# Kernel tuning notes

Measured on AMD Instinct MI355X. Metric: run time of the kernel, lower is better.

The kernel has to match this reference:

```python
import jax, jax.numpy as jnp
import numpy as np

LEAKY_SLOPE = 0.2  # alpha in the torch module
EPS = 1e-10

N_NODES = 100000
N_EDGES = 1600000
IN_F = 128
OUT_F = 64


def setup_inputs() -> dict:
    key = jax.random.key(0)
    k1, k2, k3, k4, k5 = jax.random.split(key, 5)
    h = jax.random.normal(k1, (N_NODES, IN_F), dtype=jnp.float32)
    W = jax.random.normal(k2, (IN_F, OUT_F), dtype=jnp.float32) * (1.0 / np.sqrt(IN_F))
    a1 = jax.random.normal(k3, (OUT_F,), dtype=jnp.float32) * 0.1
    a2 = jax.random.normal(k4, (OUT_F,), dtype=jnp.float32) * 0.1
    edge_index = jax.random.randint(k5, (2, N_EDGES), 0, N_NODES, dtype=jnp.int32)
    return {"h": h, "W": W, "a1": a1, "a2": a2, "edge_index": edge_index}


def reference(h, W, a1, a2, edge_index):
    # h: [N, in_f], W: [in_f, out_f], a1/a2: [out_f], edge_index: [2, E]
    N = h.shape[0]
    Wh = h @ W                                   # [N, out_f]
    row, col = edge_index[0], edge_index[1]      # [E]
    f1 = Wh @ a1                                 # [N]
    f2 = Wh @ a2                                 # [N]
    e = jax.nn.leaky_relu(f1[row] + f2[col], negative_slope=LEAKY_SLOPE)  # [E]
    e_exp = jnp.exp(e - jnp.max(e))              # global-max shift, as in torch code
    exp_sum = jax.ops.segment_sum(e_exp, row, num_segments=N)            # [N]
    alpha = e_exp / (exp_sum[row] + EPS)         # [E]  (dropout is identity in eval)
    weighted_Wh = Wh[col] * alpha[:, None]       # [E, out_f]
    h_prime = jax.ops.segment_sum(weighted_Wh, row, num_segments=N)      # [N, out_f]
    return jax.nn.elu(h_prime)                   # concat=True path
```

## Files before the change

kernel.cpp:

```cpp
#include <hip/hip_runtime.h>
#include <hip/hip_bf16.h>

#define N_NODES 100000
#define N_EDGES 1600000
#define IN_F 128
#define OUT_F 64

#define RPB 64
#define NB  1563
#define C_CHUNKS 250
#define CHUNK 6400
#define M_CNT (NB * C_CHUNKS)
#define SCANA_BLOCKS ((M_CNT + 1023) / 1024)

typedef __attribute__((ext_vector_type(8))) short short8;
typedef __attribute__((ext_vector_type(4))) float f32x4;

#define LDS_PITCH 136

__device__ __forceinline__ unsigned short f2bf(float x) {
    unsigned u = __float_as_uint(x);
    return (unsigned short)((u + 0x7FFFu + ((u >> 16) & 1u)) >> 16);
}
__device__ __forceinline__ float bf2f_u(unsigned short b) {
    return __uint_as_float((unsigned)b << 16);
}

__global__ __launch_bounds__(1024) void k_hist(
    const int* __restrict__ ei, int* __restrict__ cnt,
    const float* __restrict__ W, const float* __restrict__ a1,
    const float* __restrict__ a2, float* __restrict__ wa1, float* __restrict__ wa2)
{
    __shared__ int hl[NB];
    const int c = blockIdx.x;
    if (c == C_CHUNKS) {
        const int k = threadIdx.x;
        if (k < IN_F) {
            float s1 = 0.f, s2 = 0.f;
            #pragma unroll 8
            for (int f = 0; f < OUT_F; f++) {
                const float w = W[k * OUT_F + f];
                s1 += w * a1[f];
                s2 += w * a2[f];
            }
            wa1[k] = s1;
            wa2[k] = s2;
        }
        return;
    }
    for (int i = threadIdx.x; i < NB; i += 1024) hl[i] = 0;
    __syncthreads();
    const int e0 = c * CHUNK;
    for (int i = threadIdx.x; i < CHUNK; i += 1024)
        atomicAdd(&hl[ei[e0 + i] >> 6], 1);
    __syncthreads();
    for (int b = threadIdx.x; b < NB; b += 1024)
        cnt[b * C_CHUNKS + c] = hl[b];
}

__global__ __launch_bounds__(256) void k_gemm(
    const float* __restrict__ h, const float* __restrict__ W,
    const float* __restrict__ wa1, const float* __restrict__ wa2,
    unsigned short* __restrict__ Whb, float* __restrict__ f1, float* __restrict__ f2)
{
    __shared__ unsigned short Wt[OUT_F * LDS_PITCH];
    __shared__ unsigned short Al[16 * LDS_PITCH];

    const int tid  = threadIdx.x;
    const int lane = tid & 63;
    const int wav  = tid >> 6;
    const int quad = lane >> 4;
    const int nl   = lane & 15;

    for (int i = tid; i < IN_F * OUT_F; i += 256) {
        const int k = i >> 6, f = i & 63;
        Wt[f * LDS_PITCH + k] = f2bf(W[i]);
    }
    __syncthreads();

    short8 bfrag[4];
    #pragma unroll
    for (int ch = 0; ch < 4; ch++)
        bfrag[ch] = *(const short8*)&Wt[(wav * 16 + nl) * LDS_PITCH + ch * 32 + quad * 8];

    const int srow = tid >> 4;
    const int sc   = tid & 15;
    float w1r[8], w2r[8];
    #pragma unroll
    for (int j = 0; j < 8; j++) { w1r[j] = wa1[sc * 8 + j]; w2r[j] = wa2[sc * 8 + j]; }

    const int ntiles = N_NODES / 16;
    for (int tile = blockIdx.x; tile < ntiles; tile += gridDim.x) {
        const int base = tile * 16;
        __syncthreads();

        const float4 v0 = *(const float4*)&h[(base + srow) * IN_F + sc * 8];
        const float4 v1 = *(const float4*)&h[(base + srow) * IN_F + sc * 8 + 4];
        float p1 = v0.x * w1r[0] + v0.y * w1r[1] + v0.z * w1r[2] + v0.w * w1r[3]
                 + v1.x * w1r[4] + v1.y * w1r[5] + v1.z * w1r[6] + v1.w * w1r[7];
        float p2 = v0.x * w2r[0] + v0.y * w2r[1] + v0.z * w2r[2] + v0.w * w2r[3]
                 + v1.x * w2r[4] + v1.y * w2r[5] + v1.z * w2r[6] + v1.w * w2r[7];
        #pragma unroll
        for (int m = 8; m >= 1; m >>= 1) {
            p1 += __shfl_xor(p1, m, 64);
            p2 += __shfl_xor(p2, m, 64);
        }
        if (sc == 0) { f1[base + srow] = p1; f2[base + srow] = p2; }

        uint4 packed;
        packed.x = (unsigned)f2bf(v0.x) | ((unsigned)f2bf(v0.y) << 16);
        packed.y = (unsigned)f2bf(v0.z) | ((unsigned)f2bf(v0.w) << 16);
        packed.z = (unsigned)f2bf(v1.x) | ((unsigned)f2bf(v1.y) << 16);
        packed.w = (unsigned)f2bf(v1.z) | ((unsigned)f2bf(v1.w) << 16);
        *(uint4*)&Al[srow * LDS_PITCH + sc * 8] = packed;

        __syncthreads();

        f32x4 acc = {0.f, 0.f, 0.f, 0.f};
        #pragma unroll
        for (int ch = 0; ch < 4; ch++) {
            const short8 afrag = *(const short8*)&Al[nl * LDS_PITCH + ch * 32 + quad * 8];
            acc = __builtin_amdgcn_mfma_f32_16x16x32_bf16(afrag, bfrag[ch], acc, 0, 0, 0);
        }

        const int col = wav * 16 + nl;
        #pragma unroll
        for (int r = 0; r < 4; r++)
            Whb[(base + quad * 4 + r) * OUT_F + col] = f2bf(acc[r]);
    }
}

__global__ __launch_bounds__(256) void k_scanA(const int* __restrict__ cnt,
                                               int* __restrict__ bsum)
{
    __shared__ int sd[256];
    const int t = threadIdx.x;
    const int i0 = blockIdx.x * 1024 + t * 4;
    int s = 0;
    #pragma unroll
    for (int k = 0; k < 4; k++) {
        const int i = i0 + k;
        s += (i < M_CNT) ? cnt[i] : 0;
    }
    sd[t] = s; __syncthreads();
    for (int off = 128; off >= 1; off >>= 1) {
        if (t < off) sd[t] += sd[t + off];
        __syncthreads();
    }
    if (t == 0) bsum[blockIdx.x] = sd[0];
}

__global__ __launch_bounds__(256) void k_scanC(int* __restrict__ cnt,
                                               const int* __restrict__ bsum)
{
    __shared__ int red[256];
    __shared__ int ts[256];
    const int t = threadIdx.x;

    int pv = 0;
    for (int i = t; i < (int)blockIdx.x; i += 256) pv += bsum[i];
    red[t] = pv; __syncthreads();
    for (int off = 128; off >= 1; off >>= 1) {
        if (t < off) red[t] += red[t + off];
        __syncthreads();
    }
    const int bpref = red[0];

    const int i0 = blockIdx.x * 1024 + t * 4;
    int v[4]; int s = 0;
    #pragma unroll
    for (int k = 0; k < 4; k++) {
        const int i = i0 + k;
        v[k] = (i < M_CNT) ? cnt[i] : 0;
        s += v[k];
    }
    ts[t] = s; __syncthreads();
    for (int off = 1; off < 256; off <<= 1) {
        const int x = (t >= off) ? ts[t - off] : 0;
        __syncthreads();
        ts[t] += x;
        __syncthreads();
    }
    int excl = ts[t] - s + bpref;
    #pragma unroll
    for (int k = 0; k < 4; k++) {
        const int i = i0 + k;
        if (i < M_CNT) cnt[i] = excl;
        excl += v[k];
    }
}

__global__ __launch_bounds__(1024) void k_scatter(
    const int* __restrict__ ei,
    const float* __restrict__ f1,
    const float* __restrict__ f2,
    const int* __restrict__ cnt,
    uint2* __restrict__ pairs)
{
    __shared__ int cur[NB];
    const int c = blockIdx.x;
    for (int b = threadIdx.x; b < NB; b += 1024)
        cur[b] = cnt[b * C_CHUNKS + c];
    __syncthreads();

    const int e0 = c * CHUNK;
    for (int i = threadIdx.x; i < CHUNK; i += 1024) {
        const int r  = ei[e0 + i];
        const int cl = ei[N_EDGES + e0 + i];
        float x = f1[r] + f2[cl];
        x = (x >= 0.f) ? x : 0.2f * x;
        const float ee = __expf(x);
        const int pos = atomicAdd(&cur[r >> 6], 1);
        pairs[pos] = make_uint2(((unsigned)(r & 63) << 17) | (unsigned)cl,
                                __float_as_uint(ee));
    }
}

__global__ __launch_bounds__(256) void k_sort(
    const int* __restrict__ cnt,
    const uint2* __restrict__ pairs,
    uint2* __restrict__ pairs2,
    int* __restrict__ rowptr)
{
    __shared__ int cnt64[64];
    __shared__ int cur64[64];

    const int b   = blockIdx.x;
    const int tid = threadIdx.x;
    const int start = cnt[b * C_CHUNKS];
    const int end   = (b == NB - 1) ? N_EDGES : cnt[(b + 1) * C_CHUNKS];

    if (tid < 64) cnt64[tid] = 0;
    __syncthreads();

    for (int i = start + tid; i < end; i += 256)
        atomicAdd(&cnt64[pairs[i].x >> 17], 1);
    __syncthreads();

    if (tid < 64) {
        const int v = cnt64[tid];
        int s = v;
        #pragma unroll
        for (int off = 1; off < 64; off <<= 1) {
            const int x = __shfl_up(s, off, 64);
            if (tid >= off) s += x;
        }
        cur64[tid] = s - v;
        const int g = b * 64 + tid;
        if (g < N_NODES) rowptr[g] = start + s - v;
    }
    __syncthreads();

    for (int i = start + tid; i < end; i += 256) {
        const uint2 p = pairs[i];
        const int pos = atomicAdd(&cur64[p.x >> 17], 1);
        pairs2[start + pos] = p;
    }
    if (b == 0 && tid == 0) rowptr[N_NODES] = N_EDGES;
}

__global__ __launch_bounds__(256) void k_agg(
    const int* __restrict__ rowptr,
    const uint2* __restrict__ pairs2,
    const unsigned short* __restrict__ Whb,
    float* __restrict__ out)
{
    const int wid  = (blockIdx.x * 256 + threadIdx.x) >> 6;
    const int lane = threadIdx.x & 63;
    if (wid >= N_NODES) return;

    const int start = rowptr[wid];
    const int end   = rowptr[wid + 1];

    float acc = 0.f, s = 0.f;
    int j = start;

    for (; j + 8 <= end; j += 8) {
        uint2 p[8];
        #pragma unroll
        for (int k = 0; k < 8; k++) p[k] = pairs2[j + k];
        float wh[8];
        #pragma unroll
        for (int k = 0; k < 8; k++)
            wh[k] = bf2f_u(Whb[(((int)(p[k].x & 0x1FFFFu)) << 6) + lane]);
        #pragma unroll
        for (int k = 0; k < 8; k++) {
            const float ee = __uint_as_float(p[k].y);
            acc += ee * wh[k];
            s   += ee;
        }
    }
    for (; j + 4 <= end; j += 4) {
        uint2 p[4];
        #pragma unroll
        for (int k = 0; k < 4; k++) p[k] = pairs2[j + k];
        float wh[4];
        #pragma unroll
        for (int k = 0; k < 4; k++)
            wh[k] = bf2f_u(Whb[(((int)(p[k].x & 0x1FFFFu)) << 6) + lane]);
        #pragma unroll
        for (int k = 0; k < 4; k++) {
            const float ee = __uint_as_float(p[k].y);
            acc += ee * wh[k];
            s   += ee;
        }
    }
    for (; j < end; j++) {
        const uint2 p = pairs2[j];
        const float ee = __uint_as_float(p.y);
        acc += ee * bf2f_u(Whb[(((int)(p.x & 0x1FFFFu)) << 6) + lane]);
        s   += ee;
    }

    const float r = acc / (s + 1e-10f);
    out[wid * OUT_F + lane] = (r > 0.f) ? r : expm1f(r);
}

extern "C" void kernel_launch(void* const* d_in, const int* in_sizes, int n_in,
                              void* d_out, int out_size, void* d_ws, size_t ws_size,
                              hipStream_t stream) {
    const float* h  = (const float*)d_in[0];
    const float* W  = (const float*)d_in[1];
    const float* a1 = (const float*)d_in[2];
    const float* a2 = (const float*)d_in[3];
    const int* ei   = (const int*)d_in[4];
    float* out      = (float*)d_out;

    float* ws = (float*)d_ws;
    unsigned short* Whb = (unsigned short*)ws;
    float* f1     = ws + 3200000;
    float* f2     = f1 + N_NODES;
    float* wa1    = f2 + N_NODES;
    float* wa2    = wa1 + 128;
    int*   cnt    = (int*)(wa2 + 128);
    int*   bsum   = cnt + M_CNT;
    int*   rowptr = bsum + 384;
    int*   pad    = rowptr + 100002;
    if ((size_t)(pad - (int*)ws) & 1) pad++;
    uint2* pairs  = (uint2*)pad;
    uint2* pairs2 = pairs + N_EDGES;

    k_hist   <<<C_CHUNKS + 1, 1024, 0, stream>>>(ei, cnt, W, a1, a2, wa1, wa2);
    k_scanA  <<<SCANA_BLOCKS, 256, 0, stream>>>(cnt, bsum);
    k_scanC  <<<SCANA_BLOCKS, 256, 0, stream>>>(cnt, bsum);
    k_gemm   <<<1250, 256, 0, stream>>>(h, W, wa1, wa2, Whb, f1, f2);
    k_scatter<<<C_CHUNKS, 1024, 0, stream>>>(ei, f1, f2, cnt, pairs);
    k_sort   <<<NB, 256, 0, stream>>>(cnt, pairs, pairs2, rowptr);
    k_agg    <<<(N_NODES * 64 + 255) / 256, 256, 0, stream>>>(rowptr, pairs2, Whb, out);
}
```

Measured before the change: 228.3 us.

## Split wave into half-waves for aggregation and cache sort pairs in LDS

The aggregation kernel now has each half-wave process alternate edges, with each lane loading two bf16 features as one 32-bit word. Partial sums are combined with a cross-half shuffle, and each lane writes a float2. The intent is fewer, wider gather loads and more edges in flight per wave. The sort kernel keeps up to 2048 pairs in LDS between its count and scatter passes so the second global read is skipped, at the cost of 16KB of LDS per block, which may reduce occupancy.

```diff
diff --git a/kernel.cpp b/kernel.cpp
--- a/kernel.cpp
+++ b/kernel.cpp
@@ -12,6 +12,7 @@
 #define CHUNK 6400
 #define M_CNT (NB * C_CHUNKS)
 #define SCANA_BLOCKS ((M_CNT + 1023) / 1024)
+#define SORT_LDS_CAP 2048
 
 typedef __attribute__((ext_vector_type(8))) short short8;
 typedef __attribute__((ext_vector_type(4))) float f32x4;
@@ -222,6 +223,7 @@
     uint2* __restrict__ pairs2,
     int* __restrict__ rowptr)
 {
+    __shared__ uint2 sp[SORT_LDS_CAP];
     __shared__ int cnt64[64];
     __shared__ int cur64[64];
 
@@ -229,12 +231,16 @@
     const int tid = threadIdx.x;
     const int start = cnt[b * C_CHUNKS];
     const int end   = (b == NB - 1) ? N_EDGES : cnt[(b + 1) * C_CHUNKS];
+    const int len   = end - start;
 
     if (tid < 64) cnt64[tid] = 0;
     __syncthreads();
 
-    for (int i = start + tid; i < end; i += 256)
-        atomicAdd(&cnt64[pairs[i].x >> 17], 1);
+    for (int i = tid; i < len; i += 256) {
+        const uint2 p = pairs[start + i];
+        if (i < SORT_LDS_CAP) sp[i] = p;
+        atomicAdd(&cnt64[p.x >> 17], 1);
+    }
     __syncthreads();
 
     if (tid < 64) {
@@ -251,8 +257,8 @@
     }
     __syncthreads();
 
-    for (int i = start + tid; i < end; i += 256) {
-        const uint2 p = pairs[i];
+    for (int i = tid; i < len; i += 256) {
+        const uint2 p = (i < SORT_LDS_CAP) ? sp[i] : pairs[start + i];
         const int pos = atomicAdd(&cur64[p.x >> 17], 1);
         pairs2[start + pos] = p;
     }
@@ -272,48 +278,57 @@
     const int start = rowptr[wid];
     const int end   = rowptr[wid + 1];
 
-    float acc = 0.f, s = 0.f;
+    const int half = lane >> 5;
+    const int fl   = (lane & 31) << 1;
+
+    float acc0 = 0.f, acc1 = 0.f, s = 0.f;
     int j = start;
 
     for (; j + 8 <= end; j += 8) {
-        uint2 p[8];
-        #pragma unroll
-        for (int k = 0; k < 8; k++) p[k] = pairs2[j + k];
-        float wh[8];
-        #pragma unroll
-        for (int k = 0; k < 8; k++)
-            wh[k] = bf2f_u(Whb[(((int)(p[k].x & 0x1FFFFu)) << 6) + lane]);
-        #pragma unroll
-        for (int k = 0; k < 8; k++) {
-            const float ee = __uint_as_float(p[k].y);
-            acc += ee * wh[k];
-            s   += ee;
-        }
-    }
-    for (; j + 4 <= end; j += 4) {
         uint2 p[4];
         #pragma unroll
-        for (int k = 0; k < 4; k++) p[k] = pairs2[j + k];
-        float wh[4];
+        for (int k = 0; k < 4; k++) p[k] = pairs2[j + 2 * k + half];
+        unsigned w[4];
         #pragma unroll
         for (int k = 0; k < 4; k++)
-            wh[k] = bf2f_u(Whb[(((int)(p[k].x & 0x1FFFFu)) << 6) + lane]);
+            w[k] = *(const unsigned*)&Whb[(((int)(p[k].x & 0x1FFFFu)) << 6) + fl];
         #pragma unroll
         for (int k = 0; k < 4; k++) {
             const float ee = __uint_as_float(p[k].y);
-            acc += ee * wh[k];
-            s   += ee;
-        }
-    }
-    for (; j < end; j++) {
+            acc0 += ee * __uint_as_float(w[k] << 16);
+            acc1 += ee * __uint_as_float(w[k] & 0xFFFF0000u);
+            s    += ee;
+        }
+    }
+    for (; j + 2 <= end; j += 2) {
+        const uint2 p = pairs2[j + half];
+        const unsigned w = *(const unsigned*)&Whb[(((int)(p.x & 0x1FFFFu)) << 6) + fl];
+        const float ee = __uint_as_float(p.y);
+        acc0 += ee * __uint_as_float(w << 16);
+        acc1 += ee * __uint_as_float(w & 0xFFFF0000u);
+        s    += ee;
+    }
+    if (j < end && half == 0) {
         const uint2 p = pairs2[j];
+        const unsigned w = *(const unsigned*)&Whb[(((int)(p.x & 0x1FFFFu)) << 6) + fl];
         const float ee = __uint_as_float(p.y);
-        acc += ee * bf2f_u(Whb[(((int)(p.x & 0x1FFFFu)) << 6) + lane]);
-        s   += ee;
-    }
-
-    const float r = acc / (s + 1e-10f);
-    out[wid * OUT_F + lane] = (r > 0.f) ? r : expm1f(r);
+        acc0 += ee * __uint_as_float(w << 16);
+        acc1 += ee * __uint_as_float(w & 0xFFFF0000u);
+        s    += ee;
+    }
+
+    acc0 += __shfl_xor(acc0, 32, 64);
+    acc1 += __shfl_xor(acc1, 32, 64);
+    s    += __shfl_xor(s, 32, 64);
+
+    if (half == 0) {
+        const float inv = 1.f / (s + 1e-10f);
+        float r0 = acc0 * inv;
+        float r1 = acc1 * inv;
+        r0 = (r0 > 0.f) ? r0 : expm1f(r0);
+        r1 = (r1 > 0.f) ? r1 : expm1f(r1);
+        *(float2*)&out[wid * OUT_F + fl] = make_float2(r0, r1);
+    }
 }
 
 extern "C" void kernel_launch(void* const* d_in, const int* in_sizes, int n_in,
```

After: 229.2 us. No clear change (+0.4%).

## Stage sort bucket in LDS and software-pipeline edge loads in aggregation

Applied to the files above, without the earlier changes.

The bucket sort kernel now keeps up to 2048 pairs in shared memory during the counting pass, so the scatter pass reads them from LDS instead of reloading from global memory. The aggregation kernel prefetches the next batch of eight edge pairs while gathering Wh rows for the current batch, with masked padding replacing the 4-wide and scalar tail loops. This aims to hide the dependent pairs-then-Wh load latency and cut repeated global traffic. The cost is more registers, some wasted gathers on padded lanes, and 16KB of LDS per sort block, which may reduce occupancy.

```diff
diff --git a/kernel.cpp b/kernel.cpp
--- a/kernel.cpp
+++ b/kernel.cpp
@@ -12,6 +12,7 @@
 #define CHUNK 6400
 #define M_CNT (NB * C_CHUNKS)
 #define SCANA_BLOCKS ((M_CNT + 1023) / 1024)
+#define SORT_LDS_CAP 2048
 
 typedef __attribute__((ext_vector_type(8))) short short8;
 typedef __attribute__((ext_vector_type(4))) float f32x4;
@@ -222,6 +223,7 @@
     uint2* __restrict__ pairs2,
     int* __restrict__ rowptr)
 {
+    __shared__ uint2 sp[SORT_LDS_CAP];
     __shared__ int cnt64[64];
     __shared__ int cur64[64];
 
@@ -229,12 +231,16 @@
     const int tid = threadIdx.x;
     const int start = cnt[b * C_CHUNKS];
     const int end   = (b == NB - 1) ? N_EDGES : cnt[(b + 1) * C_CHUNKS];
+    const int len   = end - start;
 
     if (tid < 64) cnt64[tid] = 0;
     __syncthreads();
 
-    for (int i = start + tid; i < end; i += 256)
-        atomicAdd(&cnt64[pairs[i].x >> 17], 1);
+    for (int i = tid; i < len; i += 256) {
+        const uint2 p = pairs[start + i];
+        if (i < SORT_LDS_CAP) sp[i] = p;
+        atomicAdd(&cnt64[p.x >> 17], 1);
+    }
     __syncthreads();
 
     if (tid < 64) {
@@ -251,8 +257,8 @@
     }
     __syncthreads();
 
-    for (int i = start + tid; i < end; i += 256) {
-        const uint2 p = pairs[i];
+    for (int i = tid; i < len; i += 256) {
+        const uint2 p = (i < SORT_LDS_CAP) ? sp[i] : pairs[start + i];
         const int pos = atomicAdd(&cur64[p.x >> 17], 1);
         pairs2[start + pos] = p;
     }
@@ -271,45 +277,59 @@
 
     const int start = rowptr[wid];
     const int end   = rowptr[wid + 1];
+    const int deg   = end - start;
+
+    if (deg <= 0) {
+        out[wid * OUT_F + lane] = 0.f;
+        return;
+    }
+
+    const int nb = (deg + 7) >> 3;
 
     float acc = 0.f, s = 0.f;
+    uint2 p[8];
+
+    #pragma unroll
+    for (int k = 0; k < 8; k++) {
+        const int idx = start + k;
+        p[k] = pairs2[(idx < end) ? idx : (end - 1)];
+    }
+
     int j = start;
-
-    for (; j + 8 <= end; j += 8) {
-        uint2 p[8];
-        #pragma unroll
-        for (int k = 0; k < 8; k++) p[k] = pairs2[j + k];
+    for (int b = 1; b < nb; b++) {
+        const int jn = start + b * 8;
+        uint2 q[8];
+        #pragma unroll
+        for (int k = 0; k < 8; k++) {
+            const int idx = jn + k;
+            q[k] = pairs2[(idx < end) ? idx : (end - 1)];
+        }
         float wh[8];
         #pragma unroll
         for (int k = 0; k < 8; k++)
             wh[k] = bf2f_u(Whb[(((int)(p[k].x & 0x1FFFFu)) << 6) + lane]);
         #pragma unroll
         for (int k = 0; k < 8; k++) {
-            const float ee = __uint_as_float(p[k].y);
+            const float ee = (j + k < end) ? __uint_as_float(p[k].y) : 0.f;
             acc += ee * wh[k];
             s   += ee;
         }
-    }
-    for (; j + 4 <= end; j += 4) {
-        uint2 p[4];
-        #pragma unroll
-        for (int k = 0; k < 4; k++) p[k] = pairs2[j + k];
-        float wh[4];
-        #pragma unroll
-        for (int k = 0; k < 4; k++)
+        #pragma unroll
+        for (int k = 0; k < 8; k++) p[k] = q[k];
+        j = jn;
+    }
+
+    {
+        float wh[8];
+        #pragma unroll
+        for (int k = 0; k < 8; k++)
             wh[k] = bf2f_u(Whb[(((int)(p[k].x & 0x1FFFFu)) << 6) + lane]);
         #pragma unroll
-        for (int k = 0; k < 4; k++) {
-            const float ee = __uint_as_float(p[k].y);
+        for (int k = 0; k < 8; k++) {
+            const float ee = (j + k < end) ? __uint_as_float(p[k].y) : 0.f;
             acc += ee * wh[k];
             s   += ee;
         }
-    }
-    for (; j < end; j++) {
-        const uint2 p = pairs2[j];
-        const float ee = __uint_as_float(p.y);
-        acc += ee * bf2f_u(Whb[(((int)(p.x & 0x1FFFFu)) << 6) + lane]);
-        s   += ee;
     }
 
     const float r = acc / (s + 1e-10f);
```

Measured after the change: 247.1 us. 8.2% more time.
